# Kernel optimization log

Measured on AMD Instinct MI355X. Metric: run time of the kernel, lower is better.

## Reference

```python
import jax, jax.numpy as jnp
import numpy as np

T, DIM, HID = 8192, 1024, 4096

def setup_inputs() -> dict:
    key = jax.random.key(0)
    k1, k2, k3 = jax.random.split(key, 3)
    x = jax.random.normal(k1, (T, DIM), dtype=jnp.float32)
    # torch Linear weight layout: [out_features, in_features]
    W_fc = jax.random.normal(k2, (HID, DIM), dtype=jnp.float32) * 0.02
    W_proj = jax.random.normal(k3, (DIM, HID), dtype=jnp.float32) * 0.02
    return {"x": x, "W_fc": W_fc, "W_proj": W_proj}

def reference(x, W_fc, W_proj):
    # fc: x @ W_fc^T  -> relu -> square -> proj: @ W_proj^T
    h = jnp.einsum('td,hd->th', x, W_fc)      # [T, HID]
    h = jnp.square(jax.nn.relu(h))            # relu(h)^2 (relu^2 activation)
    return jnp.einsum('th,dh->td', h, W_proj) # [T, DIM]
```

## Files before the change

### kernel.cpp

```cpp
#include <hip/hip_runtime.h>
#include <stdint.h>


typedef __attribute__((ext_vector_type(8))) short bf16x8;
typedef __attribute__((ext_vector_type(4))) float f32x4;

typedef const __attribute__((address_space(1))) unsigned int* gas_u32p;
typedef __attribute__((address_space(3))) unsigned int* las_u32p;

__device__ __forceinline__ void load16_to_lds(const void* gptr, void* lptr) {
    __builtin_amdgcn_global_load_lds((gas_u32p)gptr, (las_u32p)lptr, 16, 0, 0);
}

__device__ __forceinline__ void dsr128(bf16x8& d, unsigned off) {
    asm volatile("ds_read_b128 %0, %1" : "=v"(d) : "v"(off));
}

__device__ __forceinline__ unsigned short f2bf(float f) {
    unsigned int u = __float_as_uint(f);
    u += 0x7FFFu + ((u >> 16) & 1u);
    return (unsigned short)(u >> 16);
}

#define LGKM(n) do { \
    asm volatile("s_waitcnt lgkmcnt(%0)" :: "i"(n) : "memory"); \
    __builtin_amdgcn_sched_barrier(0); } while (0)
#define VMC(n) do { \
    asm volatile("s_waitcnt vmcnt(%0)" :: "i"(n) : "memory"); \
    __builtin_amdgcn_sched_barrier(0); } while (0)

__global__ void cvt_all(const float4* __restrict__ x,  ushort4* __restrict__ xb,
                        const float4* __restrict__ wf, ushort4* __restrict__ wfb,
                        const float4* __restrict__ wp, ushort4* __restrict__ wpb)
{
    const int base = blockIdx.x * 1024 + threadIdx.x;
    #pragma unroll
    for (int j = 0; j < 4; j++) {
        const int i = base + j * 256;
        const float4* s; ushort4* d; int k;
        if (i < (1 << 21))            { s = x;  d = xb;  k = i; }
        else if (i < 3 * (1 << 20))   { s = wf; d = wfb; k = i - (1 << 21); }
        else                          { s = wp; d = wpb; k = i - 3 * (1 << 20); }
        float4 v = s[k];
        ushort4 o;
        o.x = f2bf(v.x); o.y = f2bf(v.y); o.z = f2bf(v.z); o.w = f2bf(v.w);
        d[k] = o;
    }
}

__global__ __launch_bounds__(512, 4)
void gemm_h1(const unsigned short* __restrict__ A,
             const unsigned short* __restrict__ B,
             unsigned short* __restrict__ C, int M, int N, int K)
{
    constexpr int ABYT = 8192;
    constexpr int BBYT = 16384;
    constexpr int BUFB = ABYT + BBYT;
    (void)M;

    __shared__ char lds[3 * BUFB];

    const int tid  = threadIdx.x;
    const int lane = tid & 63;
    const int wave = tid >> 6;
    const int wm   = wave >> 2;
    const int wn   = wave & 3;
    const int quad = lane >> 4;
    const int m16  = lane & 15;

    const int gx = gridDim.x;
    int flat = blockIdx.y * gx + blockIdx.x;
    const int cpx = (gx * gridDim.y) >> 3;
    flat = (flat & 7) * cpx + (flat >> 3);
    const long bm0 = (long)(flat & 63) * 128;
    const long bn0 = (long)(flat >> 6) * 256;

    const int srow   = tid >> 2;
    const int schunk = (tid & 3) ^ ((tid >> 3) & 3);
    const unsigned short* gA = A + (bm0 + srow) * (long)K + schunk * 8;
    const unsigned short* gB = B + (bn0 + srow) * (long)K + schunk * 8;

    unsigned offA[4], offB[4];
    #pragma unroll
    for (int i = 0; i < 4; i++) {
        const unsigned lo = (unsigned)((wm * 64 + i * 16 + m16) * 64 + quad * 16);
        offA[i] = lo ^ (((lo >> 7) & 3) << 4);
    }
    #pragma unroll
    for (int j = 0; j < 4; j++) {
        const unsigned lo = (unsigned)((wn * 64 + j * 16 + m16) * 64 + quad * 16);
        offB[j] = ABYT + (lo ^ (((lo >> 7) & 3) << 4));
    }

    const unsigned base =
        (unsigned)(unsigned long long)(las_u32p)(void*)lds;

    f32x4 acc[4][4];
    #pragma unroll
    for (int i = 0; i < 4; i++)
        #pragma unroll
        for (int j = 0; j < 4; j++)
            acc[i][j] = (f32x4)0.0f;

    const int NT = K >> 5;

    #define STG(po_, t_) do { \
        char* _d = (char*)lds + (po_) + tid * 16; \
        load16_to_lds(gA + (long)(t_) * 32, _d); \
        const unsigned short* _sB = gB + (long)(t_) * 32; \
        load16_to_lds(_sB, _d + ABYT); \
        load16_to_lds(_sB + 128l * K, _d + ABYT + 8192); } while (0)

    STG(0, 0);
    if (NT > 1) {
        STG(BUFB, 1);
        VMC(3);
    } else {
        VMC(0);
    }
    __builtin_amdgcn_s_barrier();

    unsigned co = 0, no = BUFB, po = 2 * BUFB;

    for (int t = 0; t < NT; ++t) {
        bf16x8 a[4], b[4];

        #pragma unroll
        for (int j = 0; j < 4; j++) dsr128(b[j], base + co + offB[j]);
        #pragma unroll
        for (int i = 0; i < 4; i++) dsr128(a[i], base + co + offA[i]);

        if (t + 2 < NT) STG(po, t + 2);

        LGKM(2);
        __builtin_amdgcn_s_setprio(1);
        #pragma unroll
        for (int i = 0; i < 2; i++)
            #pragma unroll
            for (int j = 0; j < 4; j++)
                acc[i][j] = __builtin_amdgcn_mfma_f32_16x16x32_bf16(
                    a[i], b[j], acc[i][j], 0, 0, 0);
        __builtin_amdgcn_s_setprio(0);

        LGKM(0);
        __builtin_amdgcn_s_setprio(1);
        #pragma unroll
        for (int i = 2; i < 4; i++)
            #pragma unroll
            for (int j = 0; j < 4; j++)
                acc[i][j] = __builtin_amdgcn_mfma_f32_16x16x32_bf16(
                    a[i], b[j], acc[i][j], 0, 0, 0);
        __builtin_amdgcn_s_setprio(0);

        if (t + 2 < NT) VMC(3);
        else            VMC(0);
        __builtin_amdgcn_s_barrier();

        const unsigned tmp = po; po = co; co = no; no = tmp;
    }
    #undef STG

    const long baseRow = bm0 + wm * 64 + quad * 4;
    const long baseCol = bn0 + wn * 64 + m16;
    #pragma unroll
    for (int i = 0; i < 4; i++) {
        #pragma unroll
        for (int j = 0; j < 4; j++) {
            #pragma unroll
            for (int r = 0; r < 4; r++) {
                float v = acc[i][j][r];
                v = (v > 0.0f) ? v * v : 0.0f;
                const long row = baseRow + i * 16 + r;
                const long col = baseCol + j * 16;
                C[row * (long)N + col] = f2bf(v);
            }
        }
    }
}

__global__ __launch_bounds__(512, 2)
void gemm_skew(const unsigned short* __restrict__ A,
               const unsigned short* __restrict__ B,
               float* __restrict__ C, int M, int N, int K)
{
    constexpr int AKH  = 16384;
    constexpr int BKH  = 8192;
    constexpr int BOFF = 2 * AKH;
    constexpr int BUFB = 2 * AKH + 2 * BKH;
    (void)M;

    __shared__ char lds[2 * BUFB];

    const int tid  = threadIdx.x;
    const int lane = tid & 63;
    const int wave = tid >> 6;
    const int wm   = wave >> 1;
    const int wn   = wave & 1;
    const int quad = lane >> 4;
    const int m16  = lane & 15;

    const int gx = gridDim.x;
    int flat = blockIdx.y * gx + blockIdx.x;
    const int cpx = (gx * gridDim.y) >> 3;
    flat = (flat & 7) * cpx + (flat >> 3);
    const long bm0 = (long)(flat / gx) * 256;
    const long bn0 = (long)(flat % gx) * 128;

    const int srow   = tid >> 2;
    const int schunk = (tid & 3) ^ ((tid >> 3) & 3);
    const unsigned short* gA = A + (bm0 + srow) * (long)K + schunk * 8;
    const unsigned short* gB = B + (bn0 + srow) * (long)K + schunk * 8;

    unsigned offA[4], offB[4];
    #pragma unroll
    for (int i = 0; i < 4; i++) {
        const unsigned lo = (unsigned)((wm * 64 + i * 16 + m16) * 64 + quad * 16);
        offA[i] = lo ^ (((lo >> 7) & 3) << 4);
    }
    #pragma unroll
    for (int j = 0; j < 4; j++) {
        const unsigned lo = (unsigned)((wn * 64 + j * 16 + m16) * 64 + quad * 16);
        offB[j] = lo ^ (((lo >> 7) & 3) << 4);
    }

    const unsigned ldsbase =
        (unsigned)(unsigned long long)(las_u32p)(void*)lds;

    f32x4 acc[4][4];
    #pragma unroll
    for (int i = 0; i < 4; i++)
        #pragma unroll
        for (int j = 0; j < 4; j++)
            acc[i][j] = (f32x4)0.0f;

    const int NT = K >> 6;

    #define STAGE2(t, kh) do { \
        char* _dA = (char*)lds + ((t) & 1) * BUFB + (kh) * AKH + tid * 16; \
        const unsigned short* _sA = gA + (long)(t) * 64 + (kh) * 32; \
        load16_to_lds(_sA, _dA); \
        load16_to_lds(_sA + 128l * K, _dA + 8192); \
        char* _dB = (char*)lds + ((t) & 1) * BUFB + BOFF + (kh) * BKH + tid * 16; \
        load16_to_lds(gB + (long)(t) * 64 + (kh) * 32, _dB); } while (0)

    STAGE2(0, 0); STAGE2(0, 1);
    if (NT > 1) {
        STAGE2(1, 0);
        asm volatile("s_waitcnt vmcnt(3)" ::: "memory");
    } else {
        asm volatile("s_waitcnt vmcnt(0)" ::: "memory");
    }
    __builtin_amdgcn_sched_barrier(0);
    __builtin_amdgcn_s_barrier();

    for (int t = 0; t < NT; ++t) {
        const unsigned bufo = ldsbase + (unsigned)((t & 1) * BUFB);
        bf16x8 a0[4], b0[4], a1[4], b1[4];

        #pragma unroll
        for (int i = 0; i < 4; i++) dsr128(a0[i], bufo + offA[i]);
        #pragma unroll
        for (int j = 0; j < 4; j++) dsr128(b0[j], bufo + BOFF + offB[j]);
        #pragma unroll
        for (int i = 0; i < 4; i++) dsr128(a1[i], bufo + AKH + offA[i]);
        #pragma unroll
        for (int j = 0; j < 4; j++) dsr128(b1[j], bufo + BOFF + BKH + offB[j]);
        if (t + 1 < NT) STAGE2(t + 1, 1);
        __builtin_amdgcn_s_barrier();
        asm volatile("s_waitcnt lgkmcnt(8)" ::: "memory");
        __builtin_amdgcn_sched_barrier(0);
        __builtin_amdgcn_s_setprio(1);
        #pragma unroll
        for (int i = 0; i < 4; i++)
            #pragma unroll
            for (int j = 0; j < 4; j++)
                acc[i][j] = __builtin_amdgcn_mfma_f32_16x16x32_bf16(
                    a0[i], b0[j], acc[i][j], 0, 0, 0);
        __builtin_amdgcn_s_setprio(0);
        __builtin_amdgcn_s_barrier();

        if (t + 2 < NT) STAGE2(t + 2, 0);
        asm volatile("s_waitcnt lgkmcnt(0)" ::: "memory");
        __builtin_amdgcn_sched_barrier(0);
        __builtin_amdgcn_s_setprio(1);
        #pragma unroll
        for (int i = 0; i < 4; i++)
            #pragma unroll
            for (int j = 0; j < 4; j++)
                acc[i][j] = __builtin_amdgcn_mfma_f32_16x16x32_bf16(
                    a1[i], b1[j], acc[i][j], 0, 0, 0);
        __builtin_amdgcn_s_setprio(0);
        if (t + 2 < NT) asm volatile("s_waitcnt vmcnt(3)" ::: "memory");
        else            asm volatile("s_waitcnt vmcnt(0)" ::: "memory");
        __builtin_amdgcn_sched_barrier(0);
        __builtin_amdgcn_s_barrier();
    }
    #undef STAGE2

    const long baseRow = bm0 + wm * 64 + quad * 4;
    const long baseCol = bn0 + wn * 64 + m16;
    #pragma unroll
    for (int i = 0; i < 4; i++) {
        #pragma unroll
        for (int j = 0; j < 4; j++) {
            #pragma unroll
            for (int r = 0; r < 4; r++) {
                const long row = baseRow + i * 16 + r;
                const long col = baseCol + j * 16;
                C[row * (long)N + col] = acc[i][j][r];
            }
        }
    }
}

extern "C" void kernel_launch(void* const* d_in, const int* in_sizes, int n_in,
                              void* d_out, int out_size, void* d_ws, size_t ws_size,
                              hipStream_t stream) {
    (void)in_sizes; (void)n_in; (void)out_size; (void)ws_size;

    const int T = 8192, DIM = 1024, HID = 4096;

    const float* x     = (const float*)d_in[0];
    const float* W_fc  = (const float*)d_in[1];
    const float* W_prj = (const float*)d_in[2];
    float* out = (float*)d_out;

    char* ws = (char*)d_ws;
    unsigned short* h   = (unsigned short*)ws;
    unsigned short* xb  = (unsigned short*)(ws + (64l << 20));
    unsigned short* wfb = (unsigned short*)(ws + (80l << 20));
    unsigned short* wpb = (unsigned short*)(ws + (88l << 20));

    cvt_all<<<4096, 256, 0, stream>>>(
        (const float4*)x,     (ushort4*)xb,
        (const float4*)W_fc,  (ushort4*)wfb,
        (const float4*)W_prj, (ushort4*)wpb);

    gemm_h1<<<dim3(HID / 256, T / 128), dim3(512), 0, stream>>>(
        xb, wfb, h, T, HID, DIM);

    gemm_skew<<<dim3(DIM / 128, T / 256), dim3(512), 0, stream>>>(
        h, wpb, out, T, DIM, HID);
}
```

Measured before the change: 249.0 us.

## Split-K second GEMM with 256x256 tiles and atomic accumulation

```diff
diff --git a/kernel.cpp b/kernel.cpp
--- a/kernel.cpp
+++ b/kernel.cpp
@@ -28,6 +28,7 @@
 #define VMC(n) do { \
     asm volatile("s_waitcnt vmcnt(%0)" :: "i"(n) : "memory"); \
     __builtin_amdgcn_sched_barrier(0); } while (0)
+#define LGKM0_FENCE() LGKM(0)
 
 __global__ void cvt_all(const float4* __restrict__ x,  ushort4* __restrict__ xb,
                         const float4* __restrict__ wf, ushort4* __restrict__ wfb,
@@ -179,14 +180,16 @@
 }
 
 __global__ __launch_bounds__(512, 2)
-void gemm_skew(const unsigned short* __restrict__ A,
+void gemm2_sk8(const unsigned short* __restrict__ A,
                const unsigned short* __restrict__ B,
                float* __restrict__ C, int M, int N, int K)
 {
     constexpr int AKH  = 16384;
-    constexpr int BKH  = 8192;
+    constexpr int BKH  = 16384;
     constexpr int BOFF = 2 * AKH;
     constexpr int BUFB = 2 * AKH + 2 * BKH;
+    constexpr int KEEP = 6;
+    constexpr int KW   = 2048;
     (void)M;
 
     __shared__ char lds[2 * BUFB];
@@ -194,27 +197,30 @@
     const int tid  = threadIdx.x;
     const int lane = tid & 63;
     const int wave = tid >> 6;
-    const int wm   = wave >> 1;
-    const int wn   = wave & 1;
+    const int wm   = wave >> 2;
+    const int wn   = wave & 3;
     const int quad = lane >> 4;
     const int m16  = lane & 15;
 
-    const int gx = gridDim.x;
-    int flat = blockIdx.y * gx + blockIdx.x;
-    const int cpx = (gx * gridDim.y) >> 3;
-    flat = (flat & 7) * cpx + (flat >> 3);
-    const long bm0 = (long)(flat / gx) * 256;
-    const long bn0 = (long)(flat % gx) * 128;
+    int flat = (blockIdx.z * gridDim.y + blockIdx.y) * gridDim.x + blockIdx.x;
+    flat = (flat & 7) * 32 + (flat >> 3);
+    const int  nt = flat & 3;
+    const int  mt = (flat >> 2) & 31;
+    const int  kz = flat >> 7;
+    const long bm0 = (long)mt * 256;
+    const long bn0 = (long)nt * 256;
+    const long k0  = (long)kz * KW;
 
     const int srow   = tid >> 2;
     const int schunk = (tid & 3) ^ ((tid >> 3) & 3);
-    const unsigned short* gA = A + (bm0 + srow) * (long)K + schunk * 8;
-    const unsigned short* gB = B + (bn0 + srow) * (long)K + schunk * 8;
-
-    unsigned offA[4], offB[4];
-    #pragma unroll
-    for (int i = 0; i < 4; i++) {
-        const unsigned lo = (unsigned)((wm * 64 + i * 16 + m16) * 64 + quad * 16);
+    const unsigned short* gA = A + (bm0 + srow) * (long)K + k0 + schunk * 8;
+    const unsigned short* gB = B + (bn0 + srow) * (long)K + k0 + schunk * 8;
+    char* lbase = (char*)lds;
+
+    unsigned offA[8], offB[4];
+    #pragma unroll
+    for (int i = 0; i < 8; i++) {
+        const unsigned lo = (unsigned)((wm * 128 + i * 16 + m16) * 64 + quad * 16);
         offA[i] = lo ^ (((lo >> 7) & 3) << 4);
     }
     #pragma unroll
@@ -223,91 +229,117 @@
         offB[j] = lo ^ (((lo >> 7) & 3) << 4);
     }
 
-    const unsigned ldsbase =
-        (unsigned)(unsigned long long)(las_u32p)(void*)lds;
-
-    f32x4 acc[4][4];
-    #pragma unroll
-    for (int i = 0; i < 4; i++)
+    f32x4 acc[8][4];
+    #pragma unroll
+    for (int i = 0; i < 8; i++)
         #pragma unroll
         for (int j = 0; j < 4; j++)
             acc[i][j] = (f32x4)0.0f;
 
-    const int NT = K >> 6;
-
-    #define STAGE2(t, kh) do { \
-        char* _dA = (char*)lds + ((t) & 1) * BUFB + (kh) * AKH + tid * 16; \
-        const unsigned short* _sA = gA + (long)(t) * 64 + (kh) * 32; \
-        load16_to_lds(_sA, _dA); \
-        load16_to_lds(_sA + 128l * K, _dA + 8192); \
-        char* _dB = (char*)lds + ((t) & 1) * BUFB + BOFF + (kh) * BKH + tid * 16; \
-        load16_to_lds(gB + (long)(t) * 64 + (kh) * 32, _dB); } while (0)
-
-    STAGE2(0, 0); STAGE2(0, 1);
-    if (NT > 1) {
-        STAGE2(1, 0);
-        asm volatile("s_waitcnt vmcnt(3)" ::: "memory");
-    } else {
-        asm volatile("s_waitcnt vmcnt(0)" ::: "memory");
-    }
-    __builtin_amdgcn_sched_barrier(0);
+    const int NT = KW >> 6;
+
+    #define STG_A(t, kh) do { \
+        char* _d = lbase + ((t) & 1) * BUFB + (kh) * AKH + tid * 16; \
+        const unsigned short* _s = gA + (long)(t) * 64 + (kh) * 32; \
+        load16_to_lds(_s, _d); \
+        load16_to_lds(_s + 128l * K, _d + 8192); } while (0)
+
+    #define STG_B(t, kh) do { \
+        char* _d = lbase + ((t) & 1) * BUFB + BOFF + (kh) * BKH + tid * 16; \
+        const unsigned short* _s = gB + (long)(t) * 64 + (kh) * 32; \
+        load16_to_lds(_s, _d); \
+        load16_to_lds(_s + 128l * K, _d + 8192); } while (0)
+
+    STG_B(0, 0); STG_A(0, 0); STG_B(0, 1); STG_A(0, 1);
+    STG_B(1, 0); STG_A(1, 0); STG_B(1, 1);
+    VMC(KEEP);
     __builtin_amdgcn_s_barrier();
 
     for (int t = 0; t < NT; ++t) {
-        const unsigned bufo = ldsbase + (unsigned)((t & 1) * BUFB);
-        bf16x8 a0[4], b0[4], a1[4], b1[4];
-
-        #pragma unroll
-        for (int i = 0; i < 4; i++) dsr128(a0[i], bufo + offA[i]);
-        #pragma unroll
-        for (int j = 0; j < 4; j++) dsr128(b0[j], bufo + BOFF + offB[j]);
-        #pragma unroll
-        for (int i = 0; i < 4; i++) dsr128(a1[i], bufo + AKH + offA[i]);
-        #pragma unroll
-        for (int j = 0; j < 4; j++) dsr128(b1[j], bufo + BOFF + BKH + offB[j]);
-        if (t + 1 < NT) STAGE2(t + 1, 1);
-        __builtin_amdgcn_s_barrier();
-        asm volatile("s_waitcnt lgkmcnt(8)" ::: "memory");
-        __builtin_amdgcn_sched_barrier(0);
+        char* bufA = lbase + (t & 1) * BUFB;
+        char* bufB = bufA + BOFF;
+        bf16x8 af[4], bf[4];
+
+        #pragma unroll
+        for (int j = 0; j < 4; j++) bf[j] = *(const bf16x8*)(bufB + offB[j]);
+        #pragma unroll
+        for (int i = 0; i < 4; i++) af[i] = *(const bf16x8*)(bufA + offA[i]);
+        if (t + 1 < NT) STG_A(t + 1, 1);
+        __builtin_amdgcn_s_barrier();
+        LGKM0_FENCE();
         __builtin_amdgcn_s_setprio(1);
         #pragma unroll
         for (int i = 0; i < 4; i++)
             #pragma unroll
             for (int j = 0; j < 4; j++)
                 acc[i][j] = __builtin_amdgcn_mfma_f32_16x16x32_bf16(
-                    a0[i], b0[j], acc[i][j], 0, 0, 0);
-        __builtin_amdgcn_s_setprio(0);
-        __builtin_amdgcn_s_barrier();
-
-        if (t + 2 < NT) STAGE2(t + 2, 0);
-        asm volatile("s_waitcnt lgkmcnt(0)" ::: "memory");
-        __builtin_amdgcn_sched_barrier(0);
+                    af[i], bf[j], acc[i][j], 0, 0, 0);
+        __builtin_amdgcn_s_setprio(0);
+        __builtin_amdgcn_s_barrier();
+
+        #pragma unroll
+        for (int i = 0; i < 4; i++) af[i] = *(const bf16x8*)(bufA + offA[4 + i]);
+        if (t + 2 < NT) STG_B(t + 2, 0);
+        __builtin_amdgcn_s_barrier();
+        LGKM0_FENCE();
         __builtin_amdgcn_s_setprio(1);
         #pragma unroll
         for (int i = 0; i < 4; i++)
             #pragma unroll
             for (int j = 0; j < 4; j++)
+                acc[4 + i][j] = __builtin_amdgcn_mfma_f32_16x16x32_bf16(
+                    af[i], bf[j], acc[4 + i][j], 0, 0, 0);
+        __builtin_amdgcn_s_setprio(0);
+        __builtin_amdgcn_s_barrier();
+
+        #pragma unroll
+        for (int j = 0; j < 4; j++) bf[j] = *(const bf16x8*)(bufB + BKH + offB[j]);
+        #pragma unroll
+        for (int i = 0; i < 4; i++) af[i] = *(const bf16x8*)(bufA + AKH + offA[i]);
+        if (t + 2 < NT) STG_A(t + 2, 0);
+        __builtin_amdgcn_s_barrier();
+        LGKM0_FENCE();
+        __builtin_amdgcn_s_setprio(1);
+        #pragma unroll
+        for (int i = 0; i < 4; i++)
+            #pragma unroll
+            for (int j = 0; j < 4; j++)
                 acc[i][j] = __builtin_amdgcn_mfma_f32_16x16x32_bf16(
-                    a1[i], b1[j], acc[i][j], 0, 0, 0);
-        __builtin_amdgcn_s_setprio(0);
-        if (t + 2 < NT) asm volatile("s_waitcnt vmcnt(3)" ::: "memory");
-        else            asm volatile("s_waitcnt vmcnt(0)" ::: "memory");
-        __builtin_amdgcn_sched_barrier(0);
-        __builtin_amdgcn_s_barrier();
-    }
-    #undef STAGE2
-
-    const long baseRow = bm0 + wm * 64 + quad * 4;
+                    af[i], bf[j], acc[i][j], 0, 0, 0);
+        __builtin_amdgcn_s_setprio(0);
+        __builtin_amdgcn_s_barrier();
+
+        #pragma unroll
+        for (int i = 0; i < 4; i++) af[i] = *(const bf16x8*)(bufA + AKH + offA[4 + i]);
+        if (t + 2 < NT) STG_B(t + 2, 1);
+        __builtin_amdgcn_s_barrier();
+        LGKM0_FENCE();
+        __builtin_amdgcn_s_setprio(1);
+        #pragma unroll
+        for (int i = 0; i < 4; i++)
+            #pragma unroll
+            for (int j = 0; j < 4; j++)
+                acc[4 + i][j] = __builtin_amdgcn_mfma_f32_16x16x32_bf16(
+                    af[i], bf[j], acc[4 + i][j], 0, 0, 0);
+        __builtin_amdgcn_s_setprio(0);
+        if (t + 2 < NT) VMC(KEEP);
+        else            VMC(0);
+        __builtin_amdgcn_s_barrier();
+    }
+    #undef STG_A
+    #undef STG_B
+
+    const long baseRow = bm0 + wm * 128 + quad * 4;
     const long baseCol = bn0 + wn * 64 + m16;
     #pragma unroll
-    for (int i = 0; i < 4; i++) {
+    for (int i = 0; i < 8; i++) {
         #pragma unroll
         for (int j = 0; j < 4; j++) {
             #pragma unroll
             for (int r = 0; r < 4; r++) {
                 const long row = baseRow + i * 16 + r;
                 const long col = baseCol + j * 16;
-                C[row * (long)N + col] = acc[i][j][r];
+                atomicAdd(&C[row * (long)N + col], acc[i][j][r]);
             }
         }
     }
@@ -316,7 +348,7 @@
 extern "C" void kernel_launch(void* const* d_in, const int* in_sizes, int n_in,
                               void* d_out, int out_size, void* d_ws, size_t ws_size,
                               hipStream_t stream) {
-    (void)in_sizes; (void)n_in; (void)out_size; (void)ws_size;
+    (void)in_sizes; (void)n_in; (void)ws_size;
 
     const int T = 8192, DIM = 1024, HID = 4096;
 
@@ -331,6 +363,8 @@
     unsigned short* wfb = (unsigned short*)(ws + (80l << 20));
     unsigned short* wpb = (unsigned short*)(ws + (88l << 20));
 
+    hipMemsetAsync(out, 0, (size_t)out_size, stream);
+
     cvt_all<<<4096, 256, 0, stream>>>(
         (const float4*)x,     (ushort4*)xb,
         (const float4*)W_fc,  (ushort4*)wfb,
@@ -339,6 +373,6 @@
     gemm_h1<<<dim3(HID / 256, T / 128), dim3(512), 0, stream>>>(
         xb, wfb, h, T, HID, DIM);
 
-    gemm_skew<<<dim3(DIM / 128, T / 256), dim3(512), 0, stream>>>(
+    gemm2_sk8<<<dim3(DIM / 256, T / 256, 2), dim3(512), 0, stream>>>(
         h, wpb, out, T, DIM, HID);
 }
```

Measured after the change: 284.1 us. +14.1%, slower.

## Replace pipelined 256x128 proj GEMM with single-buffered 128x128 tile kernel

Applied to the files above, without the earlier changes.

```diff
diff --git a/kernel.cpp b/kernel.cpp
--- a/kernel.cpp
+++ b/kernel.cpp
@@ -178,18 +178,14 @@
     }
 }
 
-__global__ __launch_bounds__(512, 2)
-void gemm_skew(const unsigned short* __restrict__ A,
-               const unsigned short* __restrict__ B,
-               float* __restrict__ C, int M, int N, int K)
+__global__ __launch_bounds__(256, 3)
+void gemm_p2(const unsigned short* __restrict__ A,
+             const unsigned short* __restrict__ B,
+             float* __restrict__ C, int M, int N, int K)
 {
-    constexpr int AKH  = 16384;
-    constexpr int BKH  = 8192;
-    constexpr int BOFF = 2 * AKH;
-    constexpr int BUFB = 2 * AKH + 2 * BKH;
+    __shared__ unsigned short sA[128 * 64];
+    __shared__ unsigned short sB[128 * 64];
     (void)M;
-
-    __shared__ char lds[2 * BUFB];
 
     const int tid  = threadIdx.x;
     const int lane = tid & 63;
@@ -203,29 +199,14 @@
     int flat = blockIdx.y * gx + blockIdx.x;
     const int cpx = (gx * gridDim.y) >> 3;
     flat = (flat & 7) * cpx + (flat >> 3);
-    const long bm0 = (long)(flat / gx) * 256;
+    const long bm0 = (long)(flat / gx) * 128;
     const long bn0 = (long)(flat % gx) * 128;
 
-    const int srow   = tid >> 2;
-    const int schunk = (tid & 3) ^ ((tid >> 3) & 3);
+    const int srow   = tid >> 3;
+    const int schunk = (tid & 7) ^ ((tid >> 3) & 7);
     const unsigned short* gA = A + (bm0 + srow) * (long)K + schunk * 8;
     const unsigned short* gB = B + (bn0 + srow) * (long)K + schunk * 8;
 
-    unsigned offA[4], offB[4];
-    #pragma unroll
-    for (int i = 0; i < 4; i++) {
-        const unsigned lo = (unsigned)((wm * 64 + i * 16 + m16) * 64 + quad * 16);
-        offA[i] = lo ^ (((lo >> 7) & 3) << 4);
-    }
-    #pragma unroll
-    for (int j = 0; j < 4; j++) {
-        const unsigned lo = (unsigned)((wn * 64 + j * 16 + m16) * 64 + quad * 16);
-        offB[j] = lo ^ (((lo >> 7) & 3) << 4);
-    }
-
-    const unsigned ldsbase =
-        (unsigned)(unsigned long long)(las_u32p)(void*)lds;
-
     f32x4 acc[4][4];
     #pragma unroll
     for (int i = 0; i < 4; i++)
@@ -235,67 +216,47 @@
 
     const int NT = K >> 6;
 
-    #define STAGE2(t, kh) do { \
-        char* _dA = (char*)lds + ((t) & 1) * BUFB + (kh) * AKH + tid * 16; \
-        const unsigned short* _sA = gA + (long)(t) * 64 + (kh) * 32; \
-        load16_to_lds(_sA, _dA); \
-        load16_to_lds(_sA + 128l * K, _dA + 8192); \
-        char* _dB = (char*)lds + ((t) & 1) * BUFB + BOFF + (kh) * BKH + tid * 16; \
-        load16_to_lds(gB + (long)(t) * 64 + (kh) * 32, _dB); } while (0)
-
-    STAGE2(0, 0); STAGE2(0, 1);
-    if (NT > 1) {
-        STAGE2(1, 0);
-        asm volatile("s_waitcnt vmcnt(3)" ::: "memory");
-    } else {
-        asm volatile("s_waitcnt vmcnt(0)" ::: "memory");
-    }
-    __builtin_amdgcn_sched_barrier(0);
-    __builtin_amdgcn_s_barrier();
+    #define STGP(t_) do { \
+        _Pragma("unroll") \
+        for (int c = 0; c < 4; c++) \
+            load16_to_lds(gA + (long)(c * 32) * K + (long)(t_) * 64, \
+                          (char*)sA + c * 4096 + tid * 16); \
+        _Pragma("unroll") \
+        for (int c = 0; c < 4; c++) \
+            load16_to_lds(gB + (long)(c * 32) * K + (long)(t_) * 64, \
+                          (char*)sB + c * 4096 + tid * 16); } while (0)
+
+    STGP(0);
+
+    const int rswz = (m16 & 7) << 4;
 
     for (int t = 0; t < NT; ++t) {
-        const unsigned bufo = ldsbase + (unsigned)((t & 1) * BUFB);
-        bf16x8 a0[4], b0[4], a1[4], b1[4];
-
-        #pragma unroll
-        for (int i = 0; i < 4; i++) dsr128(a0[i], bufo + offA[i]);
-        #pragma unroll
-        for (int j = 0; j < 4; j++) dsr128(b0[j], bufo + BOFF + offB[j]);
-        #pragma unroll
-        for (int i = 0; i < 4; i++) dsr128(a1[i], bufo + AKH + offA[i]);
-        #pragma unroll
-        for (int j = 0; j < 4; j++) dsr128(b1[j], bufo + BOFF + BKH + offB[j]);
-        if (t + 1 < NT) STAGE2(t + 1, 1);
-        __builtin_amdgcn_s_barrier();
-        asm volatile("s_waitcnt lgkmcnt(8)" ::: "memory");
-        __builtin_amdgcn_sched_barrier(0);
-        __builtin_amdgcn_s_setprio(1);
-        #pragma unroll
-        for (int i = 0; i < 4; i++)
+        __syncthreads();
+
+        #pragma unroll
+        for (int kh = 0; kh < 2; kh++) {
+            const int col = (kh * 64 + quad * 16) ^ rswz;
+            bf16x8 a[4], b[4];
+            #pragma unroll
+            for (int i = 0; i < 4; i++)
+                a[i] = *(const bf16x8*)((const char*)sA
+                        + (wm * 64 + i * 16 + m16) * 128 + col);
             #pragma unroll
             for (int j = 0; j < 4; j++)
-                acc[i][j] = __builtin_amdgcn_mfma_f32_16x16x32_bf16(
-                    a0[i], b0[j], acc[i][j], 0, 0, 0);
-        __builtin_amdgcn_s_setprio(0);
-        __builtin_amdgcn_s_barrier();
-
-        if (t + 2 < NT) STAGE2(t + 2, 0);
-        asm volatile("s_waitcnt lgkmcnt(0)" ::: "memory");
-        __builtin_amdgcn_sched_barrier(0);
-        __builtin_amdgcn_s_setprio(1);
-        #pragma unroll
-        for (int i = 0; i < 4; i++)
-            #pragma unroll
-            for (int j = 0; j < 4; j++)
-                acc[i][j] = __builtin_amdgcn_mfma_f32_16x16x32_bf16(
-                    a1[i], b1[j], acc[i][j], 0, 0, 0);
-        __builtin_amdgcn_s_setprio(0);
-        if (t + 2 < NT) asm volatile("s_waitcnt vmcnt(3)" ::: "memory");
-        else            asm volatile("s_waitcnt vmcnt(0)" ::: "memory");
-        __builtin_amdgcn_sched_barrier(0);
-        __builtin_amdgcn_s_barrier();
-    }
-    #undef STAGE2
+                b[j] = *(const bf16x8*)((const char*)sB
+                        + (wn * 64 + j * 16 + m16) * 128 + col);
+            #pragma unroll
+            for (int i = 0; i < 4; i++)
+                #pragma unroll
+                for (int j = 0; j < 4; j++)
+                    acc[i][j] = __builtin_amdgcn_mfma_f32_16x16x32_bf16(
+                        a[i], b[j], acc[i][j], 0, 0, 0);
+        }
+
+        __syncthreads();
+        if (t + 1 < NT) STGP(t + 1);
+    }
+    #undef STGP
 
     const long baseRow = bm0 + wm * 64 + quad * 4;
     const long baseCol = bn0 + wn * 64 + m16;
@@ -339,6 +300,6 @@
     gemm_h1<<<dim3(HID / 256, T / 128), dim3(512), 0, stream>>>(
         xb, wfb, h, T, HID, DIM);
 
-    gemm_skew<<<dim3(DIM / 128, T / 256), dim3(512), 0, stream>>>(
+    gemm_p2<<<dim3(DIM / 128, T / 128), dim3(256), 0, stream>>>(
         h, wpb, out, T, DIM, HID);
 }
```

Result: slower. 256.2 us (+2.9%).
